# Optimization experiments

Measured on AMD Instinct MI355X. Metric: run time of the kernel, lower is better.

The kernel has to match this reference:

```python
import jax, jax.numpy as jnp
import numpy as np

D = 64          # node_hidden_dim
MP_STEPS = 6    # num_step_message_passing
S2S_STEPS = 6   # num_step_set2set
LSTM_LAYERS = 3 # num_layer_set2set


def setup_inputs() -> dict:
    key = jax.random.key(0)
    ks = jax.random.split(key, 32)
    N, E, B = 10000, 50000, 500
    node_in, edge_in, edge_hid, out_dim = 15, 5, 128, 12
    s = 0.1
    inp = {}
    inp["node_feat"] = jax.random.normal(ks[0], (N, node_in), jnp.float32)
    inp["edge_feat"] = jax.random.normal(ks[1], (E, edge_in), jnp.float32)
    inp["src"] = jax.random.randint(ks[2], (E,), 0, N)
    inp["dst"] = jax.random.randint(ks[3], (E,), 0, N)
    inp["graph_ids"] = jnp.sort(jax.random.randint(ks[4], (N,), 0, B))
    inp["num_graphs"] = B
    # lin0
    inp["lin0_W"] = jax.random.normal(ks[5], (node_in, D), jnp.float32) * s
    inp["lin0_b"] = jnp.zeros((D,), jnp.float32)
    # edge network MLP (Linear -> ReLU -> Linear), output reshaped to D x D per edge
    inp["em_W1"] = jax.random.normal(ks[6], (edge_in, edge_hid), jnp.float32) * s
    inp["em_b1"] = jnp.zeros((edge_hid,), jnp.float32)
    inp["em_W2"] = jax.random.normal(ks[7], (edge_hid, D * D), jnp.float32) * 0.02
    inp["em_b2"] = jnp.zeros((D * D,), jnp.float32)
    inp["conv_bias"] = jnp.zeros((D,), jnp.float32)
    # GRU (input D, hidden D), torch layout: [3*D, in], gate order r,z,n
    inp["gru_Wih"] = jax.random.normal(ks[8], (3 * D, D), jnp.float32) * s
    inp["gru_Whh"] = jax.random.normal(ks[9], (3 * D, D), jnp.float32) * s
    inp["gru_bih"] = jnp.zeros((3 * D,), jnp.float32)
    inp["gru_bhh"] = jnp.zeros((3 * D,), jnp.float32)
    # Set2Set LSTM: input 2*D, hidden D, 3 layers. torch layout [4*D, in], gates i,f,g,o
    inp["lstm0_Wih"] = jax.random.normal(ks[10], (4 * D, 2 * D), jnp.float32) * s
    inp["lstm0_Whh"] = jax.random.normal(ks[11], (4 * D, D), jnp.float32) * s
    inp["lstm0_bih"] = jnp.zeros((4 * D,), jnp.float32)
    inp["lstm0_bhh"] = jnp.zeros((4 * D,), jnp.float32)
    inp["lstm12_Wih"] = jax.random.normal(ks[12], (2, 4 * D, D), jnp.float32) * s
    inp["lstm12_Whh"] = jax.random.normal(ks[13], (2, 4 * D, D), jnp.float32) * s
    inp["lstm12_bih"] = jnp.zeros((2, 4 * D), jnp.float32)
    inp["lstm12_bhh"] = jnp.zeros((2, 4 * D), jnp.float32)
    # output head
    inp["lin1_W"] = jax.random.normal(ks[14], (2 * D, D), jnp.float32) * s
    inp["lin1_b"] = jnp.zeros((D,), jnp.float32)
    inp["lin2_W"] = jax.random.normal(ks[15], (D, out_dim), jnp.float32) * s
    inp["lin2_b"] = jnp.zeros((out_dim,), jnp.float32)
    return inp


def _mpnn(node_feat, edge_feat, src, dst, graph_ids, num_graphs,
          lin0_W, lin0_b, em_W1, em_b1, em_W2, em_b2, conv_bias,
          gru_Wih, gru_Whh, gru_bih, gru_bhh,
          lstm0_Wih, lstm0_Whh, lstm0_bih, lstm0_bhh,
          lstm12_Wih, lstm12_Whh, lstm12_bih, lstm12_bhh,
          lin1_W, lin1_b, lin2_W, lin2_b):
    N = node_feat.shape[0]
    E = edge_feat.shape[0]
    B = num_graphs
    # initial node embedding
    out = jax.nn.relu(node_feat @ lin0_W + lin0_b)      # [N, D]
    h = out                                             # GRU hidden (seq_len=1, 1 layer)
    # per-edge weight matrices (edge features are static across steps)
    We = (jax.nn.relu(edge_feat @ em_W1 + em_b1) @ em_W2 + em_b2).reshape(E, D, D)
    for _ in range(MP_STEPS):
        # NNConv: gather src -> per-edge matvec -> scatter-add to dst
        msg = jnp.einsum('ei,eio->eo', out[src], We)    # [E, D]
        agg = jax.ops.segment_sum(msg, dst, num_segments=N) + conv_bias
        m = jax.nn.relu(agg)                            # [N, D]
        # GRU cell (torch gate order r, z, n)
        gx = m @ gru_Wih.T + gru_bih
        gh = h @ gru_Whh.T + gru_bhh
        rx, zx, nx = jnp.split(gx, 3, axis=-1)
        rh, zh, nh = jnp.split(gh, 3, axis=-1)
        r = jax.nn.sigmoid(rx + rh)
        z = jax.nn.sigmoid(zx + zh)
        n = jnp.tanh(nx + r * nh)
        h = (1.0 - z) * n + z * h
        out = h
    # Set2Set readout: 3-layer LSTM over steps, attention over nodes per graph
    h_l = [jnp.zeros((B, D), out.dtype) for _ in range(LSTM_LAYERS)]
    c_l = [jnp.zeros((B, D), out.dtype) for _ in range(LSTM_LAYERS)]
    q_star = jnp.zeros((B, 2 * D), out.dtype)
    for _ in range(S2S_STEPS):
        x = q_star
        for l in range(LSTM_LAYERS):
            if l == 0:
                Wih, Whh, bih, bhh = lstm0_Wih, lstm0_Whh, lstm0_bih, lstm0_bhh
            else:
                Wih, Whh = lstm12_Wih[l - 1], lstm12_Whh[l - 1]
                bih, bhh = lstm12_bih[l - 1], lstm12_bhh[l - 1]
            g = x @ Wih.T + bih + h_l[l] @ Whh.T + bhh
            i_g, f_g, g_g, o_g = jnp.split(g, 4, axis=-1)
            c_l[l] = jax.nn.sigmoid(f_g) * c_l[l] + jax.nn.sigmoid(i_g) * jnp.tanh(g_g)
            h_l[l] = jax.nn.sigmoid(o_g) * jnp.tanh(c_l[l])
            x = h_l[l]
        q = x                                           # [B, D]
        # segment softmax attention
        e = jnp.sum(out * q[graph_ids], axis=-1)        # [N]
        emax = jax.ops.segment_max(e, graph_ids, num_segments=B)
        ex = jnp.exp(e - emax[graph_ids])
        denom = jax.ops.segment_sum(ex, graph_ids, num_segments=B)
        alpha = ex / denom[graph_ids]                   # [N]
        readout = jax.ops.segment_sum(alpha[:, None] * out, graph_ids, num_segments=B)
        q_star = jnp.concatenate([q, readout], axis=-1) # [B, 2D]
    y = jax.nn.relu(q_star @ lin1_W + lin1_b) @ lin2_W + lin2_b
    return y


def reference(node_feat, edge_feat, src, dst, graph_ids, num_graphs,
              lin0_W, lin0_b, em_W1, em_b1, em_W2, em_b2, conv_bias,
              gru_Wih, gru_Whh, gru_bih, gru_bhh,
              lstm0_Wih, lstm0_Whh, lstm0_bih, lstm0_bhh,
              lstm12_Wih, lstm12_Whh, lstm12_bih, lstm12_bhh,
              lin1_W, lin1_b, lin2_W, lin2_b):
    return _mpnn(node_feat, edge_feat, src, dst, graph_ids, num_graphs,
                 lin0_W, lin0_b, em_W1, em_b1, em_W2, em_b2, conv_bias,
                 gru_Wih, gru_Whh, gru_bih, gru_bhh,
                 lstm0_Wih, lstm0_Whh, lstm0_bih, lstm0_bhh,
                 lstm12_Wih, lstm12_Whh, lstm12_bih, lstm12_bhh,
                 lin1_W, lin1_b, lin2_W, lin2_b)
```

## Files before the change

### kernel.cpp

```cpp
#include <hip/hip_runtime.h>
#include <math.h>

#define NGRAPH 500
#define MP_STEPS 6
#define S2S_STEPS 6
#define S2S_CAP 128

typedef _Float16 h8 __attribute__((ext_vector_type(8)));
typedef float f4 __attribute__((ext_vector_type(4)));

__device__ __forceinline__ float sigmoidf_(float v){ return 1.0f/(1.0f + expf(-v)); }

__global__ void k_zero(float* __restrict__ p, int n){
  int i = blockIdx.x*256 + threadIdx.x;
  if(i < n) p[i] = 0.f;
}

__global__ void k_lin0(const float* __restrict__ nf, const float* __restrict__ W,
                       const float* __restrict__ b, float* __restrict__ x, int N){
  int n = blockIdx.x*4 + (threadIdx.x >> 6);
  int d = threadIdx.x & 63;
  if(n >= N) return;
  float acc = b[d];
#pragma unroll
  for(int i=0;i<15;i++) acc = fmaf(nf[n*15+i], W[i*64+d], acc);
  x[n*64+d] = fmaxf(acc, 0.0f);
}

__global__ void k_edgeh(const float* __restrict__ ef, const float* __restrict__ W1,
                        const float* __restrict__ b1, _Float16* __restrict__ he, int E){
  int e = blockIdx.x;
  int h = threadIdx.x;
  if(e >= E || h >= 160) return;
  float v;
  if(h < 128){
    float acc = b1[h];
#pragma unroll
    for(int i=0;i<5;i++) acc = fmaf(ef[e*5+i], W1[i*128+h], acc);
    v = fmaxf(acc, 0.f);
  } else {
    v = (h == 128) ? 1.0f : 0.0f;
  }
  he[(size_t)e*160 + h] = (_Float16)v;
}

__global__ void k_prepW2(const float* __restrict__ W2, const float* __restrict__ b2,
                         _Float16* __restrict__ W2T){
  int idx = blockIdx.x*256 + threadIdx.x;
  if(idx >= 4096*160) return;
  int n = idx / 160, k = idx % 160;
  float v = (k < 128) ? W2[(size_t)k*4096 + n] : ((k == 128) ? b2[n] : 0.f);
  W2T[idx] = (_Float16)v;
}

__global__ __launch_bounds__(256, 2) void k_fmsg(
    const _Float16* __restrict__ he,
    const _Float16* __restrict__ W2T,
    const float* __restrict__ x,
    const int* __restrict__ src, const int* __restrict__ dst,
    float* __restrict__ agg, int E)
{
  __shared__ _Float16 hs[64*160];
  __shared__ float xsT[64*68];
  __shared__ int ds_dst[64];
  const int tid  = threadIdx.x;
  const int wave = tid >> 6;
  const int lane = tid & 63;
  const int quad = lane >> 4;
  const int l15  = lane & 15;
  const int e0   = blockIdx.x * 64;

  for(int t = tid; t < 1280; t += 256){
    int r = t / 20, c = t % 20;
    uint4 v = make_uint4(0,0,0,0);
    if(e0 + r < E) v = *(const uint4*)&he[(size_t)(e0+r)*160 + c*8];
    *(uint4*)&hs[r*160 + c*8] = v;
  }
  {
    int j = tid >> 2, qc = tid & 3;
    int sj = (e0 + j < E) ? src[e0 + j] : 0;
    const float4* xr = (const float4*)(x + (size_t)sj*64);
#pragma unroll
    for(int k=0;k<4;k++){
      float4 v = xr[qc*4 + k];
      int ib = qc*16 + k*4;
      xsT[(ib+0)*68 + j] = v.x;
      xsT[(ib+1)*68 + j] = v.y;
      xsT[(ib+2)*68 + j] = v.z;
      xsT[(ib+3)*68 + j] = v.w;
    }
  }
  if(tid < 64) ds_dst[tid] = (e0 + tid < E) ? dst[e0 + tid] : 0;
  __syncthreads();

  h8 af[4][5];
#pragma unroll
  for(int mt=0;mt<4;mt++)
#pragma unroll
    for(int ks=0;ks<5;ks++)
      af[mt][ks] = *(const h8*)&hs[(mt*16 + l15)*160 + ks*32 + (quad<<3)];

  const _Float16* bbase = W2T + ((size_t)(wave*16 + l15))*160 + (quad<<3);
  h8 bf[5], bn[5];
#pragma unroll
  for(int ks=0;ks<5;ks++) bf[ks] = *(const h8*)(bbase + ks*32);

  f4 macc[4];
#pragma unroll
  for(int mt=0;mt<4;mt++) macc[mt] = (f4){0.f,0.f,0.f,0.f};

#pragma unroll 2
  for(int i=0;i<64;i++){
    if(i < 63){
      const _Float16* nb = bbase + (size_t)(i+1)*64*160;
#pragma unroll
      for(int ks=0;ks<5;ks++) bn[ks] = *(const h8*)(nb + ks*32);
    }
    f4 g0 = (f4){0.f,0.f,0.f,0.f}, g1 = g0, g2 = g0, g3 = g0;
#pragma unroll
    for(int ks=0;ks<5;ks++){
      g0 = __builtin_amdgcn_mfma_f32_16x16x32_f16(af[0][ks], bf[ks], g0, 0, 0, 0);
      g1 = __builtin_amdgcn_mfma_f32_16x16x32_f16(af[1][ks], bf[ks], g1, 0, 0, 0);
      g2 = __builtin_amdgcn_mfma_f32_16x16x32_f16(af[2][ks], bf[ks], g2, 0, 0, 0);
      g3 = __builtin_amdgcn_mfma_f32_16x16x32_f16(af[3][ks], bf[ks], g3, 0, 0, 0);
    }
    f4 x0 = *(const f4*)&xsT[i*68 +  0 + (quad<<2)];
    f4 x1 = *(const f4*)&xsT[i*68 + 16 + (quad<<2)];
    f4 x2 = *(const f4*)&xsT[i*68 + 32 + (quad<<2)];
    f4 x3 = *(const f4*)&xsT[i*68 + 48 + (quad<<2)];
    macc[0] += x0 * g0;
    macc[1] += x1 * g1;
    macc[2] += x2 * g2;
    macc[3] += x3 * g3;
#pragma unroll
    for(int ks=0;ks<5;ks++) bf[ks] = bn[ks];
  }

  const int col = wave*16 + l15;
#pragma unroll
  for(int mt=0;mt<4;mt++){
#pragma unroll
    for(int r=0;r<4;r++){
      int edge = mt*16 + (quad<<2) + r;
      if(e0 + edge < E)
        atomicAdd(&agg[(size_t)ds_dst[edge]*64 + col], macc[mt][r]);
    }
  }
}

__global__ __launch_bounds__(256) void k_gru2(
    float* __restrict__ x, float* __restrict__ agg, const float* __restrict__ cb,
    const float* __restrict__ WihT, const float* __restrict__ WhhT,
    const float* __restrict__ bih, const float* __restrict__ bhh, int N)
{
  __shared__ float ms[32*64], hs2[32*64];
  const int tid = threadIdx.x;
  const int n0 = blockIdx.x*32;
  for(int t=tid; t<2048; t+=256){
    int n = n0 + (t>>6), d = t&63;
    float mv=0.f, hv=0.f;
    if(n < N){
      mv = fmaxf(agg[(size_t)n*64+d] + cb[d], 0.f);
      agg[(size_t)n*64+d] = 0.f;
      hv = x[(size_t)n*64+d];
    }
    ms[t]=mv; hs2[t]=hv;
  }
  __syncthreads();
  const int gx = tid & 31, ng = tid >> 5;
  float ar[4][2]={{0}}, az[4][2]={{0}}, anx[4][2]={{0}}, anh[4][2]={{0}};
#pragma unroll 4
  for(int k=0;k<64;k++){
    float wi0=WihT[k*192+gx],     wi1=WihT[k*192+gx+32];
    float wi2=WihT[k*192+gx+64],  wi3=WihT[k*192+gx+96];
    float wi4=WihT[k*192+gx+128], wi5=WihT[k*192+gx+160];
    float wh0=WhhT[k*192+gx],     wh1=WhhT[k*192+gx+32];
    float wh2=WhhT[k*192+gx+64],  wh3=WhhT[k*192+gx+96];
    float wh4=WhhT[k*192+gx+128], wh5=WhhT[k*192+gx+160];
#pragma unroll
    for(int j=0;j<4;j++){
      float mk = ms[(ng*4+j)*64+k], hk = hs2[(ng*4+j)*64+k];
      ar[j][0] = fmaf(mk,wi0, fmaf(hk,wh0, ar[j][0]));
      ar[j][1] = fmaf(mk,wi1, fmaf(hk,wh1, ar[j][1]));
      az[j][0] = fmaf(mk,wi2, fmaf(hk,wh2, az[j][0]));
      az[j][1] = fmaf(mk,wi3, fmaf(hk,wh3, az[j][1]));
      anx[j][0]= fmaf(mk,wi4, anx[j][0]);
      anx[j][1]= fmaf(mk,wi5, anx[j][1]);
      anh[j][0]= fmaf(hk,wh4, anh[j][0]);
      anh[j][1]= fmaf(hk,wh5, anh[j][1]);
    }
  }
#pragma unroll
  for(int j=0;j<4;j++){
    int n = n0 + ng*4 + j;
    if(n >= N) continue;
#pragma unroll
    for(int c=0;c<2;c++){
      int d = gx + 32*c;
      float r  = sigmoidf_(ar[j][c] + bih[d]     + bhh[d]);
      float z  = sigmoidf_(az[j][c] + bih[64+d]  + bhh[64+d]);
      float nn = tanhf(anx[j][c] + bih[128+d] + r*(anh[j][c] + bhh[128+d]));
      float hv = hs2[(ng*4+j)*64+d];
      x[(size_t)n*64+d] = (1.f - z)*nn + z*hv;
    }
  }
}

__global__ void k_tr_gru(const float* __restrict__ Wih, const float* __restrict__ Whh,
                         float* __restrict__ WihT, float* __restrict__ WhhT){
  int idx = blockIdx.x*256 + threadIdx.x;
  if(idx < 192*64){
    int r = idx/64, i = idx%64;
    WihT[i*192 + r] = Wih[idx];
    WhhT[i*192 + r] = Whh[idx];
  }
}

__global__ void k_tr_lstmcat(const float* __restrict__ w0ih, const float* __restrict__ w0hh,
                             const float* __restrict__ w12ih, const float* __restrict__ w12hh,
                             float* __restrict__ W0cat, float* __restrict__ W12cat){
  int idx = blockIdx.x*256 + threadIdx.x;
  if(idx < 192*256){
    int k = idx / 256, r = idx % 256;
    W0cat[idx] = (k < 128) ? w0ih[r*128 + k] : w0hh[r*64 + (k - 128)];
  }
  if(idx < 2*128*256){
    int l = idx / (128*256);
    int rem = idx % (128*256);
    int k = rem / 256, r = rem % 256;
    W12cat[idx] = (k < 64) ? w12ih[((size_t)l*256 + r)*64 + k]
                           : w12hh[((size_t)l*256 + r)*64 + (k - 64)];
  }
}

__device__ __forceinline__ int lbound(const int* __restrict__ a, int n, int v){
  int lo=0, hi=n;
  while(lo<hi){ int mid=(lo+hi)>>1; if(a[mid]<v) lo=mid+1; else hi=mid; }
  return lo;
}

template<int KTOT>
__device__ __forceinline__ void lstm_layer2(
    const float* __restrict__ xin, float* __restrict__ hv, float* __restrict__ cv,
    const float* __restrict__ Wcat, const float* __restrict__ bsum,
    f4* __restrict__ ps4, int t)
{
  constexpr int CH = KTOT/4;
  const int kc = t >> 6, tq = t & 63;
  const float* wp = Wcat + (size_t)(kc*CH)*256 + 4*tq;
  const float* xp = xin + kc*CH;
  f4 acc = (f4){0.f,0.f,0.f,0.f};
#pragma unroll
  for(int i=0;i<CH;i++){
    f4 w = *(const f4*)(wp + (size_t)i*256);
    acc += xp[i] * w;
  }
  ps4[t] = acc;
  __syncthreads();
  if(t < 64){
    float v[4];
#pragma unroll
    for(int g=0; g<4; g++){
      int G = g*64 + t;
      int q = G >> 2, cmp = G & 3;
      float s = 0.f;
#pragma unroll
      for(int k2=0; k2<4; k2++) s += ps4[k2*64 + q][cmp];
      v[g] = s + bsum[G];
    }
    float ig = sigmoidf_(v[0]);
    float fg = sigmoidf_(v[1]);
    float gg = tanhf(v[2]);
    float og = sigmoidf_(v[3]);
    float cn = fg*cv[t] + ig*gg;
    cv[t] = cn;
    hv[t] = og*tanhf(cn);
  }
  __syncthreads();
}

__global__ __launch_bounds__(256) void k_s2s(
    const float* __restrict__ x, const int* __restrict__ gid, int N,
    const float* __restrict__ W0cat, const float* __restrict__ W12cat,
    const float* __restrict__ l0_bih, const float* __restrict__ l0_bhh,
    const float* __restrict__ l12_bih, const float* __restrict__ l12_bhh,
    const float* __restrict__ W1, const float* __restrict__ b1,
    const float* __restrict__ W2, const float* __restrict__ b2,
    float* __restrict__ y)
{
  const int b = blockIdx.x;
  const int t = threadIdx.x;
  const int wave = t >> 6, lane = t & 63;
  __shared__ float xt[S2S_CAP*65];
  __shared__ float qcat[320];
  __shared__ float csl[192];
  __shared__ f4    ps4[256];
  __shared__ float bsum[768];
  __shared__ float ps[S2S_CAP];
  __shared__ float rop[256];
  __shared__ float wred[4], wsum[4];
  __shared__ int sh_n0, sh_n1;

  if(t == 0) sh_n0 = lbound(gid, N, b);
  if(t == 1) sh_n1 = lbound(gid, N, b+1);
  for(int i=t; i<320; i+=256) qcat[i] = 0.f;
  if(t < 192) csl[t] = 0.f;
  for(int i=t; i<768; i+=256){
    int layer = i >> 8, g = i & 255;
    float bi, bh;
    if(layer == 0){ bi = l0_bih[g]; bh = l0_bhh[g]; }
    else { bi = l12_bih[(layer-1)*256+g]; bh = l12_bhh[(layer-1)*256+g]; }
    bsum[i] = bi + bh;
  }
  __syncthreads();
  const int n0 = sh_n0, cnt = sh_n1 - sh_n0;
  const int cc = (cnt < S2S_CAP) ? cnt : S2S_CAP;

  for(int j = wave; j < cc; j += 4)
    xt[j*65 + lane] = x[(size_t)(n0+j)*64 + lane];
  __syncthreads();

  for(int step=0; step<S2S_STEPS; step++){
    lstm_layer2<192>(qcat,       qcat+128, csl,     W0cat,            bsum,       ps4, t);
    lstm_layer2<128>(qcat+128,   qcat+192, csl+64,  W12cat,           bsum+256,   ps4, t);
    lstm_layer2<128>(qcat+192,   qcat+256, csl+128, W12cat+128*256,   bsum+512,   ps4, t);

    const float* q = qcat + 256;
    float accd = 0.f;
    if(t < cc){
      const float* xr = xt + t*65;
#pragma unroll 8
      for(int k=0;k<64;k++) accd = fmaf(xr[k], q[k], accd);
    }
    float pm = (t < cc) ? accd : -1e30f;
    float qv = q[lane];
    for(int j = S2S_CAP + wave; j < cnt; j += 4){
      float p = x[(size_t)(n0+j)*64 + lane] * qv;
#pragma unroll
      for(int o=32;o;o>>=1) p += __shfl_xor(p, o, 64);
      pm = fmaxf(pm, p);
    }
#pragma unroll
    for(int o=32;o;o>>=1) pm = fmaxf(pm, __shfl_xor(pm, o, 64));
    if(lane == 0) wred[wave] = pm;
    __syncthreads();
    float mx = fmaxf(fmaxf(wred[0],wred[1]), fmaxf(wred[2],wred[3]));

    float ex = 0.f;
    if(t < cc){ ex = expf(accd - mx); ps[t] = ex; }
    float exsum = ex;
    float racc = 0.f;
    for(int j = S2S_CAP + wave; j < cnt; j += 4){
      float xv = x[(size_t)(n0+j)*64 + lane];
      float p = xv * qv;
#pragma unroll
      for(int o=32;o;o>>=1) p += __shfl_xor(p, o, 64);
      float e2 = expf(p - mx);
      if(lane == 0) exsum += e2;
      racc = fmaf(e2, xv, racc);
    }
#pragma unroll
    for(int o=32;o;o>>=1) exsum += __shfl_xor(exsum, o, 64);
    if(lane == 0) wsum[wave] = exsum;
    __syncthreads();

    for(int j = wave; j < cc; j += 4)
      racc = fmaf(ps[j], xt[j*65 + lane], racc);
    rop[wave*64 + lane] = racc;
    __syncthreads();
    if(t < 64){
      float tot = wsum[0]+wsum[1]+wsum[2]+wsum[3];
      float inv = (tot > 0.f) ? 1.f/tot : 0.f;
      float rv = (rop[t] + rop[64+t] + rop[128+t] + rop[192+t]) * inv;
      qcat[t] = qcat[256+t];
      qcat[64+t] = rv;
    }
    __syncthreads();
  }
  if(t < 64){
    float a = b1[t];
#pragma unroll 4
    for(int k=0;k<128;k++) a = fmaf(qcat[k], W1[k*64+t], a);
    rop[t] = fmaxf(a, 0.f);
  }
  __syncthreads();
  if(t < 12){
    float o = b2[t];
#pragma unroll 4
    for(int k=0;k<64;k++) o = fmaf(rop[k], W2[k*12+t], o);
    y[b*12+t] = o;
  }
}

extern "C" void kernel_launch(void* const* d_in, const int* in_sizes, int n_in,
                              void* d_out, int out_size, void* d_ws, size_t ws_size,
                              hipStream_t stream) {
  const float* node_feat = (const float*)d_in[0];
  const float* edge_feat = (const float*)d_in[1];
  const int*   src       = (const int*)d_in[2];
  const int*   dst       = (const int*)d_in[3];
  const int*   gid       = (const int*)d_in[4];
  const float* lin0_W = (const float*)d_in[6];
  const float* lin0_b = (const float*)d_in[7];
  const float* em_W1  = (const float*)d_in[8];
  const float* em_b1  = (const float*)d_in[9];
  const float* em_W2  = (const float*)d_in[10];
  const float* em_b2  = (const float*)d_in[11];
  const float* conv_b = (const float*)d_in[12];
  const float* gru_Wih = (const float*)d_in[13];
  const float* gru_Whh = (const float*)d_in[14];
  const float* gru_bih = (const float*)d_in[15];
  const float* gru_bhh = (const float*)d_in[16];
  const float* l0_Wih = (const float*)d_in[17];
  const float* l0_Whh = (const float*)d_in[18];
  const float* l0_bih = (const float*)d_in[19];
  const float* l0_bhh = (const float*)d_in[20];
  const float* l12_Wih = (const float*)d_in[21];
  const float* l12_Whh = (const float*)d_in[22];
  const float* l12_bih = (const float*)d_in[23];
  const float* l12_bhh = (const float*)d_in[24];
  const float* lin1_W = (const float*)d_in[25];
  const float* lin1_b = (const float*)d_in[26];
  const float* lin2_W = (const float*)d_in[27];
  const float* lin2_b = (const float*)d_in[28];
  float* y = (float*)d_out;

  const int N = in_sizes[0] / 15;
  const int E = in_sizes[1] / 5;
  const int B = NGRAPH;

  char* p = (char*)d_ws;
  auto carve = [&](size_t bytes)->char* {
    char* r = p; p += (bytes + 255) & ~(size_t)255; return r;
  };
  _Float16* he_h = (_Float16*)carve((size_t)E*160*2);
  _Float16* W2T  = (_Float16*)carve((size_t)4096*160*2);
  float* x      = (float*)carve((size_t)N*64*4);
  float* agg    = (float*)carve((size_t)N*64*4);
  float* gWihT  = (float*)carve(192*64*4);
  float* gWhhT  = (float*)carve(192*64*4);
  float* W0cat  = (float*)carve(192*256*4);
  float* W12cat = (float*)carve(2*128*256*4);
  (void)ws_size; (void)n_in; (void)out_size;

  k_lin0<<<(N+3)/4, 256, 0, stream>>>(node_feat, lin0_W, lin0_b, x, N);
  k_edgeh<<<E, 192, 0, stream>>>(edge_feat, em_W1, em_b1, he_h, E);
  k_prepW2<<<(4096*160+255)/256, 256, 0, stream>>>(em_W2, em_b2, W2T);
  k_tr_gru<<<(192*64+255)/256, 256, 0, stream>>>(gru_Wih, gru_Whh, gWihT, gWhhT);
  k_tr_lstmcat<<<(2*128*256+255)/256, 256, 0, stream>>>(l0_Wih, l0_Whh, l12_Wih, l12_Whh,
                                                        W0cat, W12cat);
  k_zero<<<(N*64+255)/256, 256, 0, stream>>>(agg, N*64);

  const int nblk = (E + 63) / 64;
  for(int s=0; s<MP_STEPS; s++){
    k_fmsg<<<nblk, 256, 0, stream>>>(he_h, W2T, x, src, dst, agg, E);
    k_gru2<<<(N+31)/32, 256, 0, stream>>>(x, agg, conv_b, gWihT, gWhhT, gru_bih, gru_bhh, N);
  }

  k_s2s<<<B, 256, 0, stream>>>(x, gid, N,
                               W0cat, W12cat, l0_bih, l0_bhh,
                               l12_bih, l12_bhh,
                               lin1_W, lin1_b, lin2_W, lin2_b, y);
}
```

Before: 908.4 us.

## Stream W2T fragments through per-wave LDS ring via async global_load_lds

Replaces the register double-buffered W2T B-fragment loads with an 8-slot per-wave LDS ring filled by global_load_lds, kept 7 loads ahead, with s_waitcnt vmcnt gating. The edge-hidden A fragments are now loaded straight from global memory into registers instead of being staged through shared memory. The shared footprint shrinks and register pressure drops, and occupancy is raised to 3 blocks per CU. The intent is deeper prefetch with fewer VGPRs so global-load latency is hidden behind the MFMAs. The risks are the fragile hand-written vmcnt accounting and the removal of the bounds check on the last partial edge tile. The direct A-fragment load also reads past E there.

```diff
diff --git a/kernel.cpp b/kernel.cpp
--- a/kernel.cpp
+++ b/kernel.cpp
@@ -10,6 +10,12 @@
 typedef float f4 __attribute__((ext_vector_type(4)));
 
 __device__ __forceinline__ float sigmoidf_(float v){ return 1.0f/(1.0f + expf(-v)); }
+
+__device__ __forceinline__ void gl_lds16(const _Float16* g, _Float16* l){
+  __builtin_amdgcn_global_load_lds(
+      (const __attribute__((address_space(1))) unsigned int*)g,
+      (__attribute__((address_space(3))) unsigned int*)l, 16, 0, 0);
+}
 
 __global__ void k_zero(float* __restrict__ p, int n){
   int i = blockIdx.x*256 + threadIdx.x;
@@ -53,14 +59,14 @@
   W2T[idx] = (_Float16)v;
 }
 
-__global__ __launch_bounds__(256, 2) void k_fmsg(
+__global__ __launch_bounds__(256, 3) void k_fmsg(
     const _Float16* __restrict__ he,
     const _Float16* __restrict__ W2T,
     const float* __restrict__ x,
     const int* __restrict__ src, const int* __restrict__ dst,
     float* __restrict__ agg, int E)
 {
-  __shared__ _Float16 hs[64*160];
+  __shared__ _Float16 ring[4][8][512];
   __shared__ float xsT[64*68];
   __shared__ int ds_dst[64];
   const int tid  = threadIdx.x;
@@ -70,12 +76,6 @@
   const int l15  = lane & 15;
   const int e0   = blockIdx.x * 64;
 
-  for(int t = tid; t < 1280; t += 256){
-    int r = t / 20, c = t % 20;
-    uint4 v = make_uint4(0,0,0,0);
-    if(e0 + r < E) v = *(const uint4*)&he[(size_t)(e0+r)*160 + c*8];
-    *(uint4*)&hs[r*160 + c*8] = v;
-  }
   {
     int j = tid >> 2, qc = tid & 3;
     int sj = (e0 + j < E) ? src[e0 + j] : 0;
@@ -91,38 +91,45 @@
     }
   }
   if(tid < 64) ds_dst[tid] = (e0 + tid < E) ? dst[e0 + tid] : 0;
-  __syncthreads();
 
   h8 af[4][5];
-#pragma unroll
-  for(int mt=0;mt<4;mt++)
-#pragma unroll
-    for(int ks=0;ks<5;ks++)
-      af[mt][ks] = *(const h8*)&hs[(mt*16 + l15)*160 + ks*32 + (quad<<3)];
-
-  const _Float16* bbase = W2T + ((size_t)(wave*16 + l15))*160 + (quad<<3);
-  h8 bf[5], bn[5];
-#pragma unroll
-  for(int ks=0;ks<5;ks++) bf[ks] = *(const h8*)(bbase + ks*32);
+  {
+    const _Float16* hb = he + (size_t)e0*160 + (size_t)l15*160 + quad*8;
+#pragma unroll
+    for(int mt=0;mt<4;mt++)
+#pragma unroll
+      for(int ks=0;ks<5;ks++)
+        af[mt][ks] = *(const h8*)(hb + (size_t)mt*16*160 + ks*32);
+  }
+  __syncthreads();
+
+  const _Float16* sb = W2T + ((size_t)wave*16 + l15)*160 + quad*8;
+  int nxt_i = 0, nxt_k = 0;
+#pragma unroll
+  for(int p=0;p<7;p++){
+    gl_lds16(sb + (size_t)nxt_i*10240 + nxt_k*32, &ring[wave][p][0]);
+    if(++nxt_k == 5){ nxt_k = 0; ++nxt_i; }
+  }
 
   f4 macc[4];
 #pragma unroll
   for(int mt=0;mt<4;mt++) macc[mt] = (f4){0.f,0.f,0.f,0.f};
 
-#pragma unroll 2
+  int slot = 0;
   for(int i=0;i<64;i++){
-    if(i < 63){
-      const _Float16* nb = bbase + (size_t)(i+1)*64*160;
-#pragma unroll
-      for(int ks=0;ks<5;ks++) bn[ks] = *(const h8*)(nb + ks*32);
-    }
     f4 g0 = (f4){0.f,0.f,0.f,0.f}, g1 = g0, g2 = g0, g3 = g0;
 #pragma unroll
-    for(int ks=0;ks<5;ks++){
-      g0 = __builtin_amdgcn_mfma_f32_16x16x32_f16(af[0][ks], bf[ks], g0, 0, 0, 0);
-      g1 = __builtin_amdgcn_mfma_f32_16x16x32_f16(af[1][ks], bf[ks], g1, 0, 0, 0);
-      g2 = __builtin_amdgcn_mfma_f32_16x16x32_f16(af[2][ks], bf[ks], g2, 0, 0, 0);
-      g3 = __builtin_amdgcn_mfma_f32_16x16x32_f16(af[3][ks], bf[ks], g3, 0, 0, 0);
+    for(int k=0;k<5;k++){
+      asm volatile("s_waitcnt vmcnt(6)" ::: "memory");
+      h8 bf = *(const h8*)&ring[wave][slot][lane*8];
+      int isl = (slot + 7) & 7;
+      gl_lds16(sb + (size_t)nxt_i*10240 + nxt_k*32, &ring[wave][isl][0]);
+      if(++nxt_k == 5){ nxt_k = 0; if(nxt_i < 63) ++nxt_i; }
+      slot = (slot + 1) & 7;
+      g0 = __builtin_amdgcn_mfma_f32_16x16x32_f16(af[0][k], bf, g0, 0, 0, 0);
+      g1 = __builtin_amdgcn_mfma_f32_16x16x32_f16(af[1][k], bf, g1, 0, 0, 0);
+      g2 = __builtin_amdgcn_mfma_f32_16x16x32_f16(af[2][k], bf, g2, 0, 0, 0);
+      g3 = __builtin_amdgcn_mfma_f32_16x16x32_f16(af[3][k], bf, g3, 0, 0, 0);
     }
     f4 x0 = *(const f4*)&xsT[i*68 +  0 + (quad<<2)];
     f4 x1 = *(const f4*)&xsT[i*68 + 16 + (quad<<2)];
@@ -132,8 +139,6 @@
     macc[1] += x1 * g1;
     macc[2] += x2 * g2;
     macc[3] += x3 * g3;
-#pragma unroll
-    for(int ks=0;ks<5;ks++) bf[ks] = bn[ks];
   }
 
   const int col = wave*16 + l15;
```

Result: slower. 1.179 ms (+29.8%).

## Split edge-message tile across 8 waves and drop B-fragment prefetch

Applied to the files above, without the earlier changes.

The per-edge message kernel now runs 512 threads per block, with waves split into two edge-row groups and four output-column groups, so each wave computes 32 edges by 16 columns instead of 64 by 16. This halves per-wave A fragments and accumulators and drops the software double-buffering of W2T fragments, aiming to cut register pressure and raise occupancy. The trade-off is that each W2T fragment is now loaded by two waves instead of one, and global-load latency is no longer hidden by explicit prefetch.

```diff
diff --git a/kernel.cpp b/kernel.cpp
--- a/kernel.cpp
+++ b/kernel.cpp
@@ -53,7 +53,7 @@
   W2T[idx] = (_Float16)v;
 }
 
-__global__ __launch_bounds__(256, 2) void k_fmsg(
+__global__ __launch_bounds__(512, 4) void k_fmsg(
     const _Float16* __restrict__ he,
     const _Float16* __restrict__ W2T,
     const float* __restrict__ x,
@@ -65,25 +65,27 @@
   __shared__ int ds_dst[64];
   const int tid  = threadIdx.x;
   const int wave = tid >> 6;
+  const int mg   = wave >> 2;
+  const int cg   = wave & 3;
   const int lane = tid & 63;
   const int quad = lane >> 4;
   const int l15  = lane & 15;
   const int e0   = blockIdx.x * 64;
 
-  for(int t = tid; t < 1280; t += 256){
+  for(int t = tid; t < 1280; t += 512){
     int r = t / 20, c = t % 20;
     uint4 v = make_uint4(0,0,0,0);
     if(e0 + r < E) v = *(const uint4*)&he[(size_t)(e0+r)*160 + c*8];
     *(uint4*)&hs[r*160 + c*8] = v;
   }
   {
-    int j = tid >> 2, qc = tid & 3;
+    int j = tid >> 3, oct = tid & 7;
     int sj = (e0 + j < E) ? src[e0 + j] : 0;
     const float4* xr = (const float4*)(x + (size_t)sj*64);
 #pragma unroll
-    for(int k=0;k<4;k++){
-      float4 v = xr[qc*4 + k];
-      int ib = qc*16 + k*4;
+    for(int k=0;k<2;k++){
+      float4 v = xr[oct*2 + k];
+      int ib = oct*8 + k*4;
       xsT[(ib+0)*68 + j] = v.x;
       xsT[(ib+1)*68 + j] = v.y;
       xsT[(ib+2)*68 + j] = v.z;
@@ -93,55 +95,49 @@
   if(tid < 64) ds_dst[tid] = (e0 + tid < E) ? dst[e0 + tid] : 0;
   __syncthreads();
 
-  h8 af[4][5];
-#pragma unroll
-  for(int mt=0;mt<4;mt++)
+  h8 af[2][5];
+#pragma unroll
+  for(int mt=0;mt<2;mt++)
 #pragma unroll
     for(int ks=0;ks<5;ks++)
-      af[mt][ks] = *(const h8*)&hs[(mt*16 + l15)*160 + ks*32 + (quad<<3)];
-
-  const _Float16* bbase = W2T + ((size_t)(wave*16 + l15))*160 + (quad<<3);
-  h8 bf[5], bn[5];
-#pragma unroll
-  for(int ks=0;ks<5;ks++) bf[ks] = *(const h8*)(bbase + ks*32);
-
-  f4 macc[4];
-#pragma unroll
-  for(int mt=0;mt<4;mt++) macc[mt] = (f4){0.f,0.f,0.f,0.f};
-
-#pragma unroll 2
+      af[mt][ks] = *(const h8*)&hs[(mg*32 + mt*16 + l15)*160 + ks*32 + (quad<<3)];
+
+  const _Float16* bbase = W2T + ((size_t)(cg*16 + l15))*160 + (quad<<3);
+
+  f4 macc[2];
+  macc[0] = (f4){0.f,0.f,0.f,0.f};
+  macc[1] = (f4){0.f,0.f,0.f,0.f};
+
   for(int i=0;i<64;i++){
-    if(i < 63){
-      const _Float16* nb = bbase + (size_t)(i+1)*64*160;
-#pragma unroll
-      for(int ks=0;ks<5;ks++) bn[ks] = *(const h8*)(nb + ks*32);
-    }
-    f4 g0 = (f4){0.f,0.f,0.f,0.f}, g1 = g0, g2 = g0, g3 = g0;
-#pragma unroll
-    for(int ks=0;ks<5;ks++){
-      g0 = __builtin_amdgcn_mfma_f32_16x16x32_f16(af[0][ks], bf[ks], g0, 0, 0, 0);
-      g1 = __builtin_amdgcn_mfma_f32_16x16x32_f16(af[1][ks], bf[ks], g1, 0, 0, 0);
-      g2 = __builtin_amdgcn_mfma_f32_16x16x32_f16(af[2][ks], bf[ks], g2, 0, 0, 0);
-      g3 = __builtin_amdgcn_mfma_f32_16x16x32_f16(af[3][ks], bf[ks], g3, 0, 0, 0);
-    }
-    f4 x0 = *(const f4*)&xsT[i*68 +  0 + (quad<<2)];
-    f4 x1 = *(const f4*)&xsT[i*68 + 16 + (quad<<2)];
-    f4 x2 = *(const f4*)&xsT[i*68 + 32 + (quad<<2)];
-    f4 x3 = *(const f4*)&xsT[i*68 + 48 + (quad<<2)];
+    const _Float16* bp = bbase + (size_t)i*10240;
+    h8 bf0 = *(const h8*)(bp);
+    h8 bf1 = *(const h8*)(bp + 32);
+    h8 bf2 = *(const h8*)(bp + 64);
+    h8 bf3 = *(const h8*)(bp + 96);
+    h8 bf4 = *(const h8*)(bp + 128);
+    f4 g0 = (f4){0.f,0.f,0.f,0.f}, g1 = g0;
+    g0 = __builtin_amdgcn_mfma_f32_16x16x32_f16(af[0][0], bf0, g0, 0, 0, 0);
+    g1 = __builtin_amdgcn_mfma_f32_16x16x32_f16(af[1][0], bf0, g1, 0, 0, 0);
+    g0 = __builtin_amdgcn_mfma_f32_16x16x32_f16(af[0][1], bf1, g0, 0, 0, 0);
+    g1 = __builtin_amdgcn_mfma_f32_16x16x32_f16(af[1][1], bf1, g1, 0, 0, 0);
+    g0 = __builtin_amdgcn_mfma_f32_16x16x32_f16(af[0][2], bf2, g0, 0, 0, 0);
+    g1 = __builtin_amdgcn_mfma_f32_16x16x32_f16(af[1][2], bf2, g1, 0, 0, 0);
+    g0 = __builtin_amdgcn_mfma_f32_16x16x32_f16(af[0][3], bf3, g0, 0, 0, 0);
+    g1 = __builtin_amdgcn_mfma_f32_16x16x32_f16(af[1][3], bf3, g1, 0, 0, 0);
+    g0 = __builtin_amdgcn_mfma_f32_16x16x32_f16(af[0][4], bf4, g0, 0, 0, 0);
+    g1 = __builtin_amdgcn_mfma_f32_16x16x32_f16(af[1][4], bf4, g1, 0, 0, 0);
+    f4 x0 = *(const f4*)&xsT[i*68 + mg*32 +  0 + (quad<<2)];
+    f4 x1 = *(const f4*)&xsT[i*68 + mg*32 + 16 + (quad<<2)];
     macc[0] += x0 * g0;
     macc[1] += x1 * g1;
-    macc[2] += x2 * g2;
-    macc[3] += x3 * g3;
-#pragma unroll
-    for(int ks=0;ks<5;ks++) bf[ks] = bn[ks];
-  }
-
-  const int col = wave*16 + l15;
-#pragma unroll
-  for(int mt=0;mt<4;mt++){
+  }
+
+  const int col = cg*16 + l15;
+#pragma unroll
+  for(int mt=0;mt<2;mt++){
 #pragma unroll
     for(int r=0;r<4;r++){
-      int edge = mt*16 + (quad<<2) + r;
+      int edge = mg*32 + mt*16 + (quad<<2) + r;
       if(e0 + edge < E)
         atomicAdd(&agg[(size_t)ds_dst[edge]*64 + col], macc[mt][r]);
     }
@@ -453,7 +449,7 @@
 
   const int nblk = (E + 63) / 64;
   for(int s=0; s<MP_STEPS; s++){
-    k_fmsg<<<nblk, 256, 0, stream>>>(he_h, W2T, x, src, dst, agg, E);
+    k_fmsg<<<nblk, 512, 0, stream>>>(he_h, W2T, x, src, dst, agg, E);
     k_gru2<<<(N+31)/32, 256, 0, stream>>>(x, agg, conv_b, gWihT, gWhhT, gru_bih, gru_bhh, N);
   }
 
```

Result: slower. 1.352 ms (+48.8%).
